# Kernel tuning notes

Hardware: AMD Instinct MI355X
Metric: run time of the kernel (lower is better)

## Reference

```python
import jax, jax.numpy as jnp
import numpy as np

N, E, F_IN, H, H2, G, C = 30000, 480000, 1280, 512, 256, 64, 10


def _linear_init(key, fan_in, fan_out):
    k1, k2 = jax.random.split(key)
    s = 1.0 / np.sqrt(fan_in)
    W = jax.random.uniform(k1, (fan_in, fan_out), jnp.float32, -s, s)
    b = jax.random.uniform(k2, (fan_out,), jnp.float32, -s, s)
    return W, b


def setup_inputs() -> dict:
    key = jax.random.key(0)
    ks = jax.random.split(key, 6)
    x = jax.random.normal(ks[0], (N, F_IN), jnp.float32)
    edge_index = jax.random.randint(ks[1], (2, E), 0, N, dtype=jnp.int32).astype(jnp.int64)
    batch = jnp.sort(jax.random.randint(ks[2], (N,), 0, G, dtype=jnp.int32)).astype(jnp.int64)
    W1, b1 = _linear_init(ks[3], F_IN, H)
    beta2 = jnp.ones((), jnp.float32)  # AGNNConv beta init = 1.0 (trainable in prop2)
    W2, b2 = _linear_init(ks[4], H, H2)
    W3, b3 = _linear_init(ks[5], 2 * H2, C)
    return {"x": x, "edge_index": edge_index, "batch": batch,
            "W1": W1, "b1": b1, "beta2": beta2,
            "W2": W2, "b2": b2, "W3": W3, "b3": b3}


def _agnn(x, src, dst, beta, n):
    # L2 normalize (PyG F.normalize: clamp norm at 1e-12)
    norm = jnp.maximum(jnp.linalg.norm(x, axis=-1, keepdims=True), 1e-12)
    xn = x / norm
    # per-edge cosine similarity attention logits
    alpha = beta * jnp.sum(xn[src] * xn[dst], axis=-1)  # [E']
    # softmax over incoming edges of each destination node
    amax = jax.ops.segment_max(alpha, dst, num_segments=n)
    ex = jnp.exp(alpha - amax[dst])
    denom = jax.ops.segment_sum(ex, dst, num_segments=n)
    w = ex / denom[dst]
    # weighted scatter-add of raw source features
    return jax.ops.segment_sum(w[:, None] * x[src], dst, num_segments=n)


def reference(x, edge_index, batch, W1, b1, beta2, W2, b2, W3, b3):
    n = x.shape[0]
    h = jax.nn.relu(x @ W1 + b1)  # [N, 512]
    # AGNNConv adds self-loops by default
    loops = jnp.arange(n, dtype=edge_index.dtype)
    src = jnp.concatenate([edge_index[0], loops])
    dst = jnp.concatenate([edge_index[1], loops])
    h = _agnn(h, src, dst, jnp.float32(1.0), n)  # prop1: fixed beta=1
    h = _agnn(h, src, dst, beta2, n)             # prop2: learned beta
    h = jax.nn.relu(h @ W2 + b2)  # [N, 256]
    # global max / mean pool per graph
    gmx = jax.ops.segment_max(h, batch, num_segments=G)
    cnt = jnp.maximum(jax.ops.segment_sum(jnp.ones((n,), h.dtype), batch, num_segments=G), 1.0)
    gav = jax.ops.segment_sum(h, batch, num_segments=G) / cnt[:, None]
    return jnp.concatenate([gmx, gav], axis=1) @ W3 + b3  # [G, C]
```

## Files before the change

kernel.cpp:

```cpp
#include <hip/hip_runtime.h>
#include <hip/hip_bf16.h>
#include <cstdint>


typedef __attribute__((ext_vector_type(8))) short bf16x8;
typedef __attribute__((ext_vector_type(4))) float f32x4;
typedef __attribute__((ext_vector_type(8))) unsigned short ushort8;
typedef __attribute__((ext_vector_type(4))) unsigned short ushort4v;
typedef __attribute__((ext_vector_type(4))) unsigned int uint4v;

__device__ inline unsigned short f2bf(float f) {
    unsigned int u = __float_as_uint(f);
    u += 0x7FFFu + ((u >> 16) & 1u);
    return (unsigned short)(u >> 16);
}

__device__ __forceinline__ float bf2f(unsigned short u) {
    return __uint_as_float(((unsigned int)u) << 16);
}

__device__ __forceinline__ unsigned int cvtpk(float lo, float hi) {
    unsigned int r;
    asm("v_cvt_pk_bf16_f32 %0, %1, %2" : "=v"(r) : "v"(lo), "v"(hi));
    return r;
}

__device__ __forceinline__ void gload_lds16(const void* g, void* l) {
    __builtin_amdgcn_global_load_lds(
        (const __attribute__((address_space(1))) void*)g,
        (__attribute__((address_space(3))) void*)l, 16, 0, 0);
}

__device__ __forceinline__ float wave_sum_dpp(float p) {
    int t;
    t = __builtin_amdgcn_update_dpp(0, __float_as_int(p), 0xB1, 0xf, 0xf, true);
    p += __int_as_float(t);
    t = __builtin_amdgcn_update_dpp(0, __float_as_int(p), 0x4E, 0xf, 0xf, true);
    p += __int_as_float(t);
    t = __builtin_amdgcn_update_dpp(0, __float_as_int(p), 0x141, 0xf, 0xf, true);
    p += __int_as_float(t);
    t = __builtin_amdgcn_update_dpp(0, __float_as_int(p), 0x140, 0xf, 0xf, true);
    p += __int_as_float(t);
    t = __builtin_amdgcn_update_dpp(0, __float_as_int(p), 0x142, 0xf, 0xf, true);
    p += __int_as_float(t);
    t = __builtin_amdgcn_update_dpp(0, __float_as_int(p), 0x143, 0xf, 0xf, true);
    p += __int_as_float(t);
    return __int_as_float(__builtin_amdgcn_readlane(__float_as_int(p), 63));
}

__global__ __launch_bounds__(256) void k_transpose_both(
    const float* __restrict__ W1, unsigned short* __restrict__ W1T,
    int K1, int N1, int nt1,
    const float* __restrict__ W2, unsigned short* __restrict__ W2T,
    int K2, int N2) {
    __shared__ unsigned short tb[32][33];
    int id = blockIdx.x;
    const float* W; unsigned short* Wt; int K, N, bx, by;
    if (id < nt1) {
        W = W1; Wt = W1T; K = K1; N = N1;
        int nx = K1 / 32; bx = id % nx; by = id / nx;
    } else {
        id -= nt1;
        W = W2; Wt = W2T; K = K2; N = N2;
        int nx = K2 / 32; bx = id % nx; by = id / nx;
    }
    int k0 = bx * 32, n0 = by * 32;
    int tr = threadIdx.x >> 3;
    int tc = (threadIdx.x & 7) * 4;
    float4 v = *(const float4*)(W + (long)(k0 + tr) * N + n0 + tc);
    tb[tr][tc + 0] = f2bf(v.x); tb[tr][tc + 1] = f2bf(v.y);
    tb[tr][tc + 2] = f2bf(v.z); tb[tr][tc + 3] = f2bf(v.w);
    __syncthreads();
    ushort4v o = { tb[tc + 0][tr], tb[tc + 1][tr], tb[tc + 2][tr], tb[tc + 3][tr] };
    *(ushort4v*)(Wt + (long)(n0 + tr) * K + k0 + tc) = o;
}

template <int K, int BN, int NOUT, bool AF32, bool OUTBF16>
__global__ __launch_bounds__(512, 4) void k_gemm_bias_relu(
    const void* __restrict__ Av, const unsigned short* __restrict__ Bt,
    const float* __restrict__ bias, void* __restrict__ Cv, int M) {
    constexpr int NSTEP = K / 32;
    constexpr int NF = BN / 64;
    __shared__ unsigned short As[2][128 * 32];
    __shared__ unsigned short Bs[2][BN * 32];
    int tid = threadIdx.x;
    int w = tid >> 6, l = tid & 63;
    int wm = w >> 2, wn = w & 3;
    int mBase = blockIdx.x * 128;
    int nBase = blockIdx.y * BN;

    const float* Af = (const float*)Av;
    const unsigned short* Ab = (const unsigned short*)Av;

    int arow = tid >> 2;
    int aslot = (tid & 3) ^ ((arow >> 1) & 3);
    long aRowG = mBase + arow; if (aRowG >= M) aRowG = M - 1;
    const float* aptr = AF32 ? (Af + aRowG * K + (tid & 3) * 8) : nullptr;

    auto stageB = [&](int b, int k0) {
#pragma unroll
        for (int o = 0; o < BN / 128; ++o) {
            int rbase = (w * (BN / 128) + o) * 16;
            int row = rbase + (l >> 2);
            int gsrc = (l & 3) ^ ((row >> 1) & 3);
            gload_lds16(Bt + (long)(nBase + row) * K + k0 + gsrc * 8,
                        &Bs[b][rbase * 32]);
        }
    };
    auto stageAbf = [&](int b, int k0) {
        int rbase = w * 16;
        int row = rbase + (l >> 2);
        int gsrc = (l & 3) ^ ((row >> 1) & 3);
        long gr = mBase + row; if (gr >= M) gr = M - 1;
        gload_lds16(Ab + gr * K + k0 + gsrc * 8, &As[b][rbase * 32]);
    };

    f32x4 acc[4][NF] = {};

    stageB(0, 0);
    if constexpr (AF32) {
        float4 z0 = *(const float4*)(aptr);
        float4 z1 = *(const float4*)(aptr + 4);
        uint4v p = { cvtpk(z0.x, z0.y), cvtpk(z0.z, z0.w),
                     cvtpk(z1.x, z1.y), cvtpk(z1.z, z1.w) };
        *(uint4v*)(&As[0][arow * 32 + aslot * 8]) = p;
    } else {
        stageAbf(0, 0);
    }
    __syncthreads();

    int s = 0;
    for (int step = 0; step < NSTEP; ++step, s ^= 1) {
        int nk = (step + 1) * 32;
        float4 f0, f1;
        if (nk < K) {
            stageB(s ^ 1, nk);
            if constexpr (AF32) {
                f0 = *(const float4*)(aptr + nk);
                f1 = *(const float4*)(aptr + nk + 4);
            } else {
                stageAbf(s ^ 1, nk);
            }
        }
        bf16x8 af[4];
#pragma unroll
        for (int m = 0; m < 4; ++m) {
            int ra = wm * 64 + m * 16 + (l & 15);
            int g = (l >> 4) ^ ((ra >> 1) & 3);
            af[m] = *(const bf16x8*)(&As[s][ra * 32 + g * 8]);
        }
#pragma unroll
        for (int n = 0; n < NF; ++n) {
            int rb = wn * (BN / 4) + n * 16 + (l & 15);
            int g = (l >> 4) ^ ((rb >> 1) & 3);
            bf16x8 bfr = *(const bf16x8*)(&Bs[s][rb * 32 + g * 8]);
#pragma unroll
            for (int m = 0; m < 4; ++m)
                acc[m][n] = __builtin_amdgcn_mfma_f32_16x16x32_bf16(
                    af[m], bfr, acc[m][n], 0, 0, 0);
        }
        if constexpr (AF32) {
            if (nk < K) {
                uint4v p = { cvtpk(f0.x, f0.y), cvtpk(f0.z, f0.w),
                             cvtpk(f1.x, f1.y), cvtpk(f1.z, f1.w) };
                *(uint4v*)(&As[s ^ 1][arow * 32 + aslot * 8]) = p;
            }
        }
        __syncthreads();
    }

#pragma unroll
    for (int m = 0; m < 4; ++m) {
        int row = mBase + wm * 64 + m * 16 + (l >> 4) * 4;
#pragma unroll
        for (int n = 0; n < NF; ++n) {
            int colg = nBase + wn * (BN / 4) + n * 16 + (l & 15);
            float bv = bias[colg];
#pragma unroll
            for (int r = 0; r < 4; ++r) {
                if (row + r < M) {
                    float v = fmaxf(acc[m][n][r] + bv, 0.f);
                    if constexpr (OUTBF16)
                        ((unsigned short*)Cv)[(long)(row + r) * NOUT + colg] = f2bf(v);
                    else
                        ((float*)Cv)[(long)(row + r) * NOUT + colg] = v;
                }
            }
        }
    }
}

__global__ void k_csr_init(int* __restrict__ cnt, int* __restrict__ fill, int n) {
    int i = blockIdx.x * blockDim.x + threadIdx.x;
    if (i < n) { cnt[i] = 1; fill[i] = 0; }
}

__global__ void k_csr_count(const int* __restrict__ ei, int* __restrict__ cnt, int E) {
    int e = blockIdx.x * blockDim.x + threadIdx.x;
    if (e < E) atomicAdd(&cnt[ei[E + e]], 1);
}

__global__ __launch_bounds__(1024) void k_scan1(const int* __restrict__ cnt,
                                                int* __restrict__ rowp,
                                                int* __restrict__ bsum, int n) {
    __shared__ int wsum[16];
    int b = blockIdx.x, t = threadIdx.x, lane = t & 63, w = t >> 6;
    int i = b * 1024 + t;
    int v = (i < n) ? cnt[i] : 0;
    int x = v;
#pragma unroll
    for (int off = 1; off < 64; off <<= 1) {
        int y = __shfl_up(x, off, 64);
        if (lane >= off) x += y;
    }
    if (lane == 63) wsum[w] = x;
    __syncthreads();
    if (t < 16) {
        int s = wsum[t];
#pragma unroll
        for (int off = 1; off < 16; off <<= 1) {
            int y = __shfl_up(s, off, 64);
            if (t >= off) s += y;
        }
        wsum[t] = s;
    }
    __syncthreads();
    int wo = w ? wsum[w - 1] : 0;
    if (i < n) rowp[i] = wo + x - v;
    if (t == 0) bsum[b] = wsum[15];
}

__global__ __launch_bounds__(1024) void k_scan23(const int* __restrict__ bsum,
                                                 int* __restrict__ rowp, int n, int nb) {
    __shared__ int off[65];
    int t = threadIdx.x;
    if (t < 64) {
        int v = (t < nb) ? bsum[t] : 0;
        int x = v;
#pragma unroll
        for (int o = 1; o < 64; o <<= 1) {
            int y = __shfl_up(x, o, 64);
            if (t >= o) x += y;
        }
        off[t] = x - v;
        if (t == nb - 1) off[64] = x;
    }
    __syncthreads();
    int i = blockIdx.x * 1024 + t;
    if (i < n) rowp[i] += off[i >> 10];
    else if (i == n) rowp[n] = off[64];
}

__global__ void k_csr_fill(const int* __restrict__ ei, const int* __restrict__ rowp,
                           int* __restrict__ fill, int* __restrict__ col, int E, int n) {
    int idx = blockIdx.x * blockDim.x + threadIdx.x;
    if (idx < E) {
        int d = ei[E + idx];
        int s = ei[idx];
        int pos = atomicAdd(&fill[d], 1);
        col[rowp[d] + pos] = s;
    } else if (idx < E + n) {
        int nd = idx - E;
        int pos = atomicAdd(&fill[nd], 1);
        col[rowp[nd] + pos] = nd;
    }
}

__global__ __launch_bounds__(256) void k_norm_bf16(const unsigned short* __restrict__ h,
                                                   float* __restrict__ invn, int n) {
    int row = blockIdx.x * 4 + (threadIdx.x >> 6);
    int lane = threadIdx.x & 63;
    if (row >= n) return;
    ushort8 v = *(const ushort8*)(h + (long)row * 512 + lane * 8);
    float s = 0.f;
#pragma unroll
    for (int e = 0; e < 8; ++e) { float f = bf2f(v[e]); s += f * f; }
    s = wave_sum_dpp(s);
    if (lane == 0) invn[row] = 1.f / fmaxf(sqrtf(s), 1e-12f);
}

__global__ __launch_bounds__(256) void k_agnn(
    const unsigned short* __restrict__ h, const float* __restrict__ invn,
    const int* __restrict__ rowp, const int* __restrict__ col,
    const float* __restrict__ beta_ptr, unsigned short* __restrict__ out,
    float* __restrict__ invn_out, int nNodes) {
    int dst = blockIdx.x * 4 + (threadIdx.x >> 6);
    int lane = threadIdx.x & 63;
    if (dst >= nNodes) return;
    float beta = beta_ptr ? beta_ptr[0] : 1.0f;
    ushort8 hdv = *(const ushort8*)(h + (long)dst * 512 + lane * 8);
    float hd[8];
#pragma unroll
    for (int e = 0; e < 8; ++e) hd[e] = bf2f(hdv[e]);
    float coef = beta * invn[dst];
    float mshift = fabsf(beta) * 1.0625f;
    int s0 = rowp[dst], s1 = rowp[dst + 1];

    float ssum = 0.f;
    float accE[8] = {0.f, 0.f, 0.f, 0.f, 0.f, 0.f, 0.f, 0.f};
    float accO[8] = {0.f, 0.f, 0.f, 0.f, 0.f, 0.f, 0.f, 0.f};

    for (int base = s0; base < s1; base += 64) {
        int cnt = min(s1 - base, 64);
        int gi = base + lane; if (gi >= s1) gi = s1 - 1;
        int idxl = col[gi];
        float vinl = invn[idxl];
        ushort8 r0 = {}, r1 = {}, r2 = {}, r3 = {};
        r0 = *(const ushort8*)(h + (long)__builtin_amdgcn_readlane(idxl, 0) * 512 + lane * 8);
        if (cnt > 1) r1 = *(const ushort8*)(h + (long)__builtin_amdgcn_readlane(idxl, 1) * 512 + lane * 8);
        if (cnt > 2) r2 = *(const ushort8*)(h + (long)__builtin_amdgcn_readlane(idxl, 2) * 512 + lane * 8);
        if (cnt > 3) r3 = *(const ushort8*)(h + (long)__builtin_amdgcn_readlane(idxl, 3) * 512 + lane * 8);
        int j = 0;
        for (; j + 1 < cnt; j += 2) {
            ushort8 c0 = r0, c1 = r1;
            r0 = r2; r1 = r3;
            if (j + 4 < cnt) r2 = *(const ushort8*)(h + (long)__builtin_amdgcn_readlane(idxl, j + 4) * 512 + lane * 8);
            if (j + 5 < cnt) r3 = *(const ushort8*)(h + (long)__builtin_amdgcn_readlane(idxl, j + 5) * 512 + lane * 8);
            float a0[8], a1[8];
#pragma unroll
            for (int e = 0; e < 8; ++e) { a0[e] = bf2f(c0[e]); a1[e] = bf2f(c1[e]); }
            float p0 = a0[0] * hd[0] + a0[1] * hd[1] + a0[2] * hd[2] + a0[3] * hd[3] +
                       a0[4] * hd[4] + a0[5] * hd[5] + a0[6] * hd[6] + a0[7] * hd[7];
            float p1 = a1[0] * hd[0] + a1[1] * hd[1] + a1[2] * hd[2] + a1[3] * hd[3] +
                       a1[4] * hd[4] + a1[5] * hd[5] + a1[6] * hd[6] + a1[7] * hd[7];
            p0 = wave_sum_dpp(p0);
            p1 = wave_sum_dpp(p1);
            float al0 = coef * __int_as_float(__builtin_amdgcn_readlane(__float_as_int(vinl), j)) * p0;
            float al1 = coef * __int_as_float(__builtin_amdgcn_readlane(__float_as_int(vinl), j + 1)) * p1;
            float w0 = __expf(al0 - mshift);
            float w1 = __expf(al1 - mshift);
            ssum += w0 + w1;
#pragma unroll
            for (int e = 0; e < 8; ++e) { accE[e] += w0 * a0[e]; accO[e] += w1 * a1[e]; }
        }
        if (j < cnt) {
            float a0[8];
#pragma unroll
            for (int e = 0; e < 8; ++e) a0[e] = bf2f(r0[e]);
            float p0 = a0[0] * hd[0] + a0[1] * hd[1] + a0[2] * hd[2] + a0[3] * hd[3] +
                       a0[4] * hd[4] + a0[5] * hd[5] + a0[6] * hd[6] + a0[7] * hd[7];
            p0 = wave_sum_dpp(p0);
            float al0 = coef * __int_as_float(__builtin_amdgcn_readlane(__float_as_int(vinl), j)) * p0;
            float w0 = __expf(al0 - mshift);
            ssum += w0;
#pragma unroll
            for (int e = 0; e < 8; ++e) accE[e] += w0 * a0[e];
        }
    }
    float inv_s = 1.f / ssum;
    float acc[8];
#pragma unroll
    for (int e = 0; e < 8; ++e) acc[e] = (accE[e] + accO[e]) * inv_s;

    uint4v o = { cvtpk(acc[0], acc[1]), cvtpk(acc[2], acc[3]),
                 cvtpk(acc[4], acc[5]), cvtpk(acc[6], acc[7]) };
    *(uint4v*)(out + (long)dst * 512 + lane * 8) = o;

    if (invn_out) {
        float s = 0.f;
#pragma unroll
        for (int e = 0; e < 8; ++e) s += acc[e] * acc[e];
        s = wave_sum_dpp(s);
        if (lane == 0) invn_out[dst] = 1.f / fmaxf(sqrtf(s), 1e-12f);
    }
}

__global__ __launch_bounds__(256) void k_pool(const unsigned short* __restrict__ h3,
                                              const int* __restrict__ batch,
                                              float* __restrict__ pooled, int n) {
    __shared__ int se[2];
    int g = blockIdx.x;
    if (threadIdx.x < 2) {
        int tgt = g + (int)threadIdx.x;
        int lo = 0, hi = n;
        while (lo < hi) {
            int mid = (lo + hi) >> 1;
            if (batch[mid] < tgt) lo = mid + 1; else hi = mid;
        }
        se[threadIdx.x] = lo;
    }
    __syncthreads();
    int s = se[0], e = se[1];
    int t = threadIdx.x;
    float mx = -3.402823466e38f, sm = 0.f;
    int r = s;
    for (; r + 4 <= e; r += 4) {
        float v0 = bf2f(h3[(long)(r + 0) * 256 + t]);
        float v1 = bf2f(h3[(long)(r + 1) * 256 + t]);
        float v2 = bf2f(h3[(long)(r + 2) * 256 + t]);
        float v3 = bf2f(h3[(long)(r + 3) * 256 + t]);
        mx = fmaxf(mx, fmaxf(fmaxf(v0, v1), fmaxf(v2, v3)));
        sm += (v0 + v1) + (v2 + v3);
    }
    for (; r < e; ++r) {
        float v = bf2f(h3[(long)r * 256 + t]);
        mx = fmaxf(mx, v); sm += v;
    }
    float cnt = fmaxf((float)(e - s), 1.f);
    pooled[g * 512 + t] = mx;
    pooled[g * 512 + 256 + t] = sm / cnt;
}

__global__ __launch_bounds__(64) void k_final(const float* __restrict__ pooled,
                                              const float* __restrict__ W3,
                                              const float* __restrict__ b3,
                                              float* __restrict__ out, int C) {
    int g = blockIdx.x;
    int lane = threadIdx.x;
    for (int c = 0; c < C; c++) {
        float p = 0.f;
        for (int k = lane; k < 512; k += 64) p += pooled[g * 512 + k] * W3[k * C + c];
#pragma unroll
        for (int off = 32; off; off >>= 1) p += __shfl_xor(p, off, 64);
        if (lane == 0) out[g * C + c] = p + b3[c];
    }
}

extern "C" void kernel_launch(void* const* d_in, const int* in_sizes, int n_in,
                              void* d_out, int out_size, void* d_ws, size_t ws_size,
                              hipStream_t stream) {
    const float* x     = (const float*)d_in[0];
    const int*   ei    = (const int*)d_in[1];
    const int*   batch = (const int*)d_in[2];
    const float* W1    = (const float*)d_in[3];
    const float* b1    = (const float*)d_in[4];
    const float* beta2 = (const float*)d_in[5];
    const float* W2    = (const float*)d_in[6];
    const float* b2    = (const float*)d_in[7];
    const float* W3    = (const float*)d_in[8];
    const float* b3    = (const float*)d_in[9];
    float* out = (float*)d_out;

    const int N = in_sizes[2];
    const int E = in_sizes[1] / 2;
    const int F_IN = in_sizes[0] / N;
    const int H = in_sizes[4];
    const int H2 = in_sizes[7];
    const int C = in_sizes[9];
    const int G = out_size / C;

    char* ws = (char*)d_ws;
    unsigned short* H1B = (unsigned short*)(ws + 0);
    unsigned short* H3B = (unsigned short*)(ws + 0);
    unsigned short* HPB = (unsigned short*)(ws + 31000000L);
    unsigned short* H2B = (unsigned short*)(ws + 62000000L);
    unsigned short* W1T = (unsigned short*)(ws + 93000000L);
    unsigned short* W2T = (unsigned short*)(ws + 94500000L);
    float* INVN_A = (float*)(ws + 95000000L);
    float* INVN_B = (float*)(ws + 95200000L);
    int*   CNT    = (int*)(ws + 95400000L);
    int*   FILL   = (int*)(ws + 95600000L);
    int*   ROWP   = (int*)(ws + 95800000L);
    int*   COL    = (int*)(ws + 96000000L);
    int*   BSUM   = (int*)(ws + 98100000L);
    float* POOLED = (float*)(ws + 98120000L);

    int nt1 = (F_IN / 32) * (H / 32);
    int nt2 = (H / 32) * (H2 / 32);
    k_transpose_both<<<nt1 + nt2, 256, 0, stream>>>(W1, W1T, F_IN, H, nt1,
                                                    W2, W2T, H, H2);

    int nb = (N + 1023) / 1024;
    k_csr_init<<<(N + 255) / 256, 256, 0, stream>>>(CNT, FILL, N);
    k_csr_count<<<(E + 255) / 256, 256, 0, stream>>>(ei, CNT, E);
    k_scan1<<<nb, 1024, 0, stream>>>(CNT, ROWP, BSUM, N);
    k_scan23<<<(N + 1 + 1023) / 1024, 1024, 0, stream>>>(BSUM, ROWP, N, nb);
    k_csr_fill<<<(E + N + 255) / 256, 256, 0, stream>>>(ei, ROWP, FILL, COL, E, N);

    {
        dim3 grid((N + 127) / 128, H / 256);
        k_gemm_bias_relu<1280, 256, 512, true, true>
            <<<grid, 512, 0, stream>>>(x, W1T, b1, H1B, N);
    }

    k_norm_bf16<<<(N + 3) / 4, 256, 0, stream>>>(H1B, INVN_A, N);
    k_agnn<<<(N + 3) / 4, 256, 0, stream>>>(H1B, INVN_A, ROWP, COL, nullptr, HPB, INVN_B, N);

    k_agnn<<<(N + 3) / 4, 256, 0, stream>>>(HPB, INVN_B, ROWP, COL, beta2, H2B, nullptr, N);

    {
        dim3 grid((N + 127) / 128, H2 / 128);
        k_gemm_bias_relu<512, 128, 256, false, true>
            <<<grid, 512, 0, stream>>>(H2B, W2T, b2, H3B, N);
    }

    k_pool<<<G, 256, 0, stream>>>(H3B, batch, POOLED, N);
    k_final<<<G, 64, 0, stream>>>(POOLED, W3, b3, out, C);
}
```

Before: 353.1 us.

## Fuse row-norm into GEMM1 epilogue, merge pool with final linear, drop init kernel

The first GEMM epilogue now computes per-row partial sums of squares of the ReLU outputs. It reduces them across 16 lanes with DPP and writes them to a small buffer. A tiny kernel then turns these into inverse norms, replacing the separate pass that re-read H1 to normalize. GEMM1's N tile shrinks from 256 to 128, which doubles the grid but also means the fp32 input is re-read more times. Separately, the CSR init kernel is replaced by a memset with the self-loop count folded into the scan, and pooling is fused with the final linear layer.

```diff
diff --git a/kernel.cpp b/kernel.cpp
--- a/kernel.cpp
+++ b/kernel.cpp
@@ -46,6 +46,19 @@
     t = __builtin_amdgcn_update_dpp(0, __float_as_int(p), 0x143, 0xf, 0xf, true);
     p += __int_as_float(t);
     return __int_as_float(__builtin_amdgcn_readlane(__float_as_int(p), 63));
+}
+
+__device__ __forceinline__ float row16_sum_dpp(float p) {
+    int t;
+    t = __builtin_amdgcn_update_dpp(0, __float_as_int(p), 0xB1, 0xf, 0xf, true);
+    p += __int_as_float(t);
+    t = __builtin_amdgcn_update_dpp(0, __float_as_int(p), 0x4E, 0xf, 0xf, true);
+    p += __int_as_float(t);
+    t = __builtin_amdgcn_update_dpp(0, __float_as_int(p), 0x141, 0xf, 0xf, true);
+    p += __int_as_float(t);
+    t = __builtin_amdgcn_update_dpp(0, __float_as_int(p), 0x140, 0xf, 0xf, true);
+    p += __int_as_float(t);
+    return p;
 }
 
 __global__ __launch_bounds__(256) void k_transpose_both(
@@ -75,10 +88,11 @@
     *(ushort4v*)(Wt + (long)(n0 + tr) * K + k0 + tc) = o;
 }
 
-template <int K, int BN, int NOUT, bool AF32, bool OUTBF16>
+template <int K, int BN, int NOUT, bool AF32, bool OUTBF16, bool PSUM_EN>
 __global__ __launch_bounds__(512, 4) void k_gemm_bias_relu(
     const void* __restrict__ Av, const unsigned short* __restrict__ Bt,
-    const float* __restrict__ bias, void* __restrict__ Cv, int M) {
+    const float* __restrict__ bias, void* __restrict__ Cv,
+    float* __restrict__ psum, int M) {
     constexpr int NSTEP = K / 32;
     constexpr int NF = BN / 64;
     __shared__ unsigned short As[2][128 * 32];
@@ -99,8 +113,8 @@
 
     auto stageB = [&](int b, int k0) {
 #pragma unroll
-        for (int o = 0; o < BN / 128; ++o) {
-            int rbase = (w * (BN / 128) + o) * 16;
+        for (int o = 0; o < (BN + 127) / 128; ++o) {
+            int rbase = (w * ((BN + 127) / 128) + o) * 16;
             int row = rbase + (l >> 2);
             int gsrc = (l & 3) ^ ((row >> 1) & 3);
             gload_lds16(Bt + (long)(nBase + row) * K + k0 + gsrc * 8,
@@ -169,30 +183,46 @@
         __syncthreads();
     }
 
+    float bv[NF];
+#pragma unroll
+    for (int n = 0; n < NF; ++n)
+        bv[n] = bias[nBase + wn * (BN / 4) + n * 16 + (l & 15)];
 #pragma unroll
     for (int m = 0; m < 4; ++m) {
-        int row = mBase + wm * 64 + m * 16 + (l >> 4) * 4;
-#pragma unroll
-        for (int n = 0; n < NF; ++n) {
-            int colg = nBase + wn * (BN / 4) + n * 16 + (l & 15);
-            float bv = bias[colg];
-#pragma unroll
-            for (int r = 0; r < 4; ++r) {
-                if (row + r < M) {
-                    float v = fmaxf(acc[m][n][r] + bv, 0.f);
+#pragma unroll
+        for (int r = 0; r < 4; ++r) {
+            int row = mBase + wm * 64 + m * 16 + (l >> 4) * 4 + r;
+            float sq = 0.f;
+#pragma unroll
+            for (int n = 0; n < NF; ++n) {
+                float v = fmaxf(acc[m][n][r] + bv[n], 0.f);
+                sq += v * v;
+                if (row < M) {
+                    int colg = nBase + wn * (BN / 4) + n * 16 + (l & 15);
                     if constexpr (OUTBF16)
-                        ((unsigned short*)Cv)[(long)(row + r) * NOUT + colg] = f2bf(v);
+                        ((unsigned short*)Cv)[(long)row * NOUT + colg] = f2bf(v);
                     else
-                        ((float*)Cv)[(long)(row + r) * NOUT + colg] = v;
+                        ((float*)Cv)[(long)row * NOUT + colg] = v;
                 }
             }
-        }
-    }
-}
-
-__global__ void k_csr_init(int* __restrict__ cnt, int* __restrict__ fill, int n) {
-    int i = blockIdx.x * blockDim.x + threadIdx.x;
-    if (i < n) { cnt[i] = 1; fill[i] = 0; }
+            if constexpr (PSUM_EN) {
+                sq = row16_sum_dpp(sq);
+                if ((l & 15) == 0 && row < M)
+                    psum[(long)row * 16 + blockIdx.y * 4 + wn] = sq;
+            }
+        }
+    }
+}
+
+__global__ void k_rsqrt(const float* __restrict__ psum,
+                        float* __restrict__ invn, int n) {
+    int i = blockIdx.x * 256 + threadIdx.x;
+    if (i >= n) return;
+    const float4* p = (const float4*)(psum + (long)i * 16);
+    float4 a = p[0], b = p[1], c = p[2], d = p[3];
+    float s = (a.x + a.y + a.z + a.w) + (b.x + b.y + b.z + b.w) +
+              (c.x + c.y + c.z + c.w) + (d.x + d.y + d.z + d.w);
+    invn[i] = 1.f / fmaxf(sqrtf(s), 1e-12f);
 }
 
 __global__ void k_csr_count(const int* __restrict__ ei, int* __restrict__ cnt, int E) {
@@ -206,7 +236,7 @@
     __shared__ int wsum[16];
     int b = blockIdx.x, t = threadIdx.x, lane = t & 63, w = t >> 6;
     int i = b * 1024 + t;
-    int v = (i < n) ? cnt[i] : 0;
+    int v = (i < n) ? cnt[i] + 1 : 0;
     int x = v;
 #pragma unroll
     for (int off = 1; off < 64; off <<= 1) {
@@ -264,19 +294,6 @@
         int pos = atomicAdd(&fill[nd], 1);
         col[rowp[nd] + pos] = nd;
     }
-}
-
-__global__ __launch_bounds__(256) void k_norm_bf16(const unsigned short* __restrict__ h,
-                                                   float* __restrict__ invn, int n) {
-    int row = blockIdx.x * 4 + (threadIdx.x >> 6);
-    int lane = threadIdx.x & 63;
-    if (row >= n) return;
-    ushort8 v = *(const ushort8*)(h + (long)row * 512 + lane * 8);
-    float s = 0.f;
-#pragma unroll
-    for (int e = 0; e < 8; ++e) { float f = bf2f(v[e]); s += f * f; }
-    s = wave_sum_dpp(s);
-    if (lane == 0) invn[row] = 1.f / fmaxf(sqrtf(s), 1e-12f);
 }
 
 __global__ __launch_bounds__(256) void k_agnn(
@@ -365,23 +382,25 @@
     }
 }
 
-__global__ __launch_bounds__(256) void k_pool(const unsigned short* __restrict__ h3,
-                                              const int* __restrict__ batch,
-                                              float* __restrict__ pooled, int n) {
+__global__ __launch_bounds__(256) void k_pool_final(
+    const unsigned short* __restrict__ h3, const int* __restrict__ batch,
+    const float* __restrict__ W3, const float* __restrict__ b3,
+    float* __restrict__ out, int n, int C) {
     __shared__ int se[2];
+    __shared__ float wpart[4];
     int g = blockIdx.x;
-    if (threadIdx.x < 2) {
-        int tgt = g + (int)threadIdx.x;
+    int t = threadIdx.x;
+    if (t < 2) {
+        int tgt = g + t;
         int lo = 0, hi = n;
         while (lo < hi) {
             int mid = (lo + hi) >> 1;
             if (batch[mid] < tgt) lo = mid + 1; else hi = mid;
         }
-        se[threadIdx.x] = lo;
+        se[t] = lo;
     }
     __syncthreads();
     int s = se[0], e = se[1];
-    int t = threadIdx.x;
     float mx = -3.402823466e38f, sm = 0.f;
     int r = s;
     for (; r + 4 <= e; r += 4) {
@@ -397,22 +416,15 @@
         mx = fmaxf(mx, v); sm += v;
     }
     float cnt = fmaxf((float)(e - s), 1.f);
-    pooled[g * 512 + t] = mx;
-    pooled[g * 512 + 256 + t] = sm / cnt;
-}
-
-__global__ __launch_bounds__(64) void k_final(const float* __restrict__ pooled,
-                                              const float* __restrict__ W3,
-                                              const float* __restrict__ b3,
-                                              float* __restrict__ out, int C) {
-    int g = blockIdx.x;
-    int lane = threadIdx.x;
-    for (int c = 0; c < C; c++) {
-        float p = 0.f;
-        for (int k = lane; k < 512; k += 64) p += pooled[g * 512 + k] * W3[k * C + c];
-#pragma unroll
-        for (int off = 32; off; off >>= 1) p += __shfl_xor(p, off, 64);
-        if (lane == 0) out[g * C + c] = p + b3[c];
+    float av = sm / cnt;
+    for (int c = 0; c < C; ++c) {
+        float part = mx * W3[(long)t * C + c] + av * W3[(long)(256 + t) * C + c];
+        part = wave_sum_dpp(part);
+        if ((t & 63) == 0) wpart[t >> 6] = part;
+        __syncthreads();
+        if (t == 0)
+            out[g * C + c] = wpart[0] + wpart[1] + wpart[2] + wpart[3] + b3[c];
+        __syncthreads();
     }
 }
 
@@ -453,7 +465,9 @@
     int*   ROWP   = (int*)(ws + 95800000L);
     int*   COL    = (int*)(ws + 96000000L);
     int*   BSUM   = (int*)(ws + 98100000L);
-    float* POOLED = (float*)(ws + 98120000L);
+    float* PSUM   = (float*)(ws + 98110000L);
+
+    hipMemsetAsync(ws + 95400000L, 0, 400000, stream);
 
     int nt1 = (F_IN / 32) * (H / 32);
     int nt2 = (H / 32) * (H2 / 32);
@@ -461,29 +475,27 @@
                                                     W2, W2T, H, H2);
 
     int nb = (N + 1023) / 1024;
-    k_csr_init<<<(N + 255) / 256, 256, 0, stream>>>(CNT, FILL, N);
     k_csr_count<<<(E + 255) / 256, 256, 0, stream>>>(ei, CNT, E);
     k_scan1<<<nb, 1024, 0, stream>>>(CNT, ROWP, BSUM, N);
     k_scan23<<<(N + 1 + 1023) / 1024, 1024, 0, stream>>>(BSUM, ROWP, N, nb);
     k_csr_fill<<<(E + N + 255) / 256, 256, 0, stream>>>(ei, ROWP, FILL, COL, E, N);
 
     {
-        dim3 grid((N + 127) / 128, H / 256);
-        k_gemm_bias_relu<1280, 256, 512, true, true>
-            <<<grid, 512, 0, stream>>>(x, W1T, b1, H1B, N);
-    }
-
-    k_norm_bf16<<<(N + 3) / 4, 256, 0, stream>>>(H1B, INVN_A, N);
+        dim3 grid((N + 127) / 128, H / 128);
+        k_gemm_bias_relu<1280, 128, 512, true, true, true>
+            <<<grid, 512, 0, stream>>>(x, W1T, b1, H1B, PSUM, N);
+    }
+    k_rsqrt<<<(N + 255) / 256, 256, 0, stream>>>(PSUM, INVN_A, N);
+
     k_agnn<<<(N + 3) / 4, 256, 0, stream>>>(H1B, INVN_A, ROWP, COL, nullptr, HPB, INVN_B, N);
 
     k_agnn<<<(N + 3) / 4, 256, 0, stream>>>(HPB, INVN_B, ROWP, COL, beta2, H2B, nullptr, N);
 
     {
         dim3 grid((N + 127) / 128, H2 / 128);
-        k_gemm_bias_relu<512, 128, 256, false, true>
-            <<<grid, 512, 0, stream>>>(H2B, W2T, b2, H3B, N);
-    }
-
-    k_pool<<<G, 256, 0, stream>>>(H3B, batch, POOLED, N);
-    k_final<<<G, 64, 0, stream>>>(POOLED, W3, b3, out, C);
-}
+        k_gemm_bias_relu<512, 128, 256, false, true, false>
+            <<<grid, 512, 0, stream>>>(H2B, W2T, b2, H3B, nullptr, N);
+    }
+
+    k_pool_final<<<G, 256, 0, stream>>>(H3B, batch, W3, b3, out, N, C);
+}
```

Result: slower. 393.6 us (+11.5%).
